# Performance work log

Measured on AMD Instinct MI355X. Metric: run time of the kernel, lower is better.

Reference implementation:

```python
import jax, jax.numpy as jnp
import numpy as np

EMBED_DIM = 1024
NUM_HEADS = 16
HEAD_DIM = EMBED_DIM // NUM_HEADS
CACHE_LEN = 16384


def setup_inputs() -> dict:
    key = jax.random.key(0)
    ks = jax.random.split(key, 10)
    s = 1.0 / np.sqrt(EMBED_DIM)
    return {
        "x": jax.random.normal(ks[0], (EMBED_DIM,), dtype=jnp.float32),
        "vk_cache": jax.random.normal(ks[1], (2, CACHE_LEN, NUM_HEADS, HEAD_DIM), dtype=jnp.float32),
        "Wv": jax.random.normal(ks[2], (EMBED_DIM, EMBED_DIM), dtype=jnp.float32) * s,
        "bv": jnp.zeros((EMBED_DIM,), dtype=jnp.float32),
        "Wq": jax.random.normal(ks[3], (EMBED_DIM, EMBED_DIM), dtype=jnp.float32) * s,
        "bq": jnp.zeros((EMBED_DIM,), dtype=jnp.float32),
        "Wk": jax.random.normal(ks[4], (EMBED_DIM, EMBED_DIM), dtype=jnp.float32) * s,
        "bk": jnp.zeros((EMBED_DIM,), dtype=jnp.float32),
        "Wo": jax.random.normal(ks[5], (EMBED_DIM, EMBED_DIM), dtype=jnp.float32) * s,
        "bo": jnp.zeros((EMBED_DIM,), dtype=jnp.float32),
    }


def reference(x, vk_cache, Wv, bv, Wq, bq, Wk, bk, Wo, bo):
    # Project single token to q/k/v
    v_i = (x @ Wv + bv).reshape(1, NUM_HEADS, HEAD_DIM)
    q_i = (x @ Wq + bq).reshape(NUM_HEADS, HEAD_DIM)
    k_i = (x @ Wk + bk).reshape(1, NUM_HEADS, HEAD_DIM)
    # Shift cache left by one, append new token   -> (CACHE_LEN, H, D)
    v = jnp.concatenate((vk_cache[0, 1:], v_i), axis=0)
    k = jnp.concatenate((vk_cache[1, 1:], k_i), axis=0)
    # Valid positions = any nonzero value entry
    mask = jnp.any(v != 0, axis=(1, 2))  # (CACHE_LEN,)
    # Scaled dot-product attention for the single query
    att = jnp.einsum('hd,khd->hk', q_i, k) / jnp.sqrt(jnp.float32(HEAD_DIM))
    att = jnp.where(mask, att, -jnp.inf)
    att = jax.nn.softmax(att, axis=-1)
    values = jnp.einsum('hk,khd->hd', att, v).reshape(EMBED_DIM)
    out_i = values @ Wo + bo
    return (out_i, jnp.stack([v, k]))
```

## Files before the change

### kernel.cpp

```cpp
#include <hip/hip_runtime.h>
#include <math.h>

#define EMBED 1024
#define NHEAD 16
#define HDIM  64
#define CLEN  16384

#define WS_QKV   0
#define WS_QP    3072
#define WS_PM    199680
#define WS_PL    216064
#define WS_PACC  232448
#define WS_GM    1281024
#define WS_GL    1281536
#define WS_GACC  1282048
#define WS_OPART 1314816

__global__ __launch_bounds__(256) void qkv_proj(
    const float* __restrict__ x,
    const float* __restrict__ Wq,
    const float* __restrict__ Wk,
    const float* __restrict__ Wv,
    float* __restrict__ ws) {
  int m = blockIdx.x >> 6;
  int c = blockIdx.x & 63;
  const float* W = (m == 0) ? Wq : (m == 1) ? Wk : Wv;
  int j = threadIdx.x << 2;
  int i0 = c * 16;
  float4 acc = make_float4(0.f, 0.f, 0.f, 0.f);
  for (int i = i0; i < i0 + 16; ++i) {
    float xv = x[i];
    float4 w = *(const float4*)(W + (size_t)i * EMBED + j);
    acc.x += xv * w.x; acc.y += xv * w.y;
    acc.z += xv * w.z; acc.w += xv * w.w;
  }
  *(float4*)(ws + WS_QP + (size_t)(m * 64 + c) * EMBED + j) = acc;
}

__global__ __launch_bounds__(256) void qkv_reduce(
    const float* __restrict__ bq, const float* __restrict__ bk,
    const float* __restrict__ bv, float* __restrict__ ws) {
  int m = blockIdx.x >> 2;
  int j = ((blockIdx.x & 3) << 8) + threadIdx.x;
  const float* b = (m == 0) ? bq : (m == 1) ? bk : bv;
  float s = b[j];
  const float* p = ws + WS_QP + (size_t)m * 64 * EMBED + j;
  for (int c = 0; c < 64; ++c) s += p[(size_t)c * EMBED];
  ws[WS_QKV + m * EMBED + j] = s;
}

__global__ __launch_bounds__(256) void shift_attn(
    const float* __restrict__ cache,
    float* __restrict__ out,
    float* __restrict__ ws) {
  __shared__ float sacc[3][EMBED];
  __shared__ float sm[4][NHEAD];
  __shared__ float sl[4][NHEAD];

  const int wv   = threadIdx.x >> 6;
  const int lane = threadIdx.x & 63;
  const int grp  = lane >> 4;

  float qf[16];
#pragma unroll
  for (int c = 0; c < 4; ++c) {
    float4 t = *(const float4*)(ws + WS_QKV + c * 256 + lane * 4);
    qf[c * 4] = t.x; qf[c * 4 + 1] = t.y; qf[c * 4 + 2] = t.z; qf[c * 4 + 3] = t.w;
  }

  float m[4] = {-INFINITY, -INFINITY, -INFINITY, -INFINITY};
  float l[4] = {0.f, 0.f, 0.f, 0.f};
  float acc[16];
#pragma unroll
  for (int j = 0; j < 16; ++j) acc[j] = 0.f;

  const float* vin = cache;
  const float* kin = cache + (size_t)CLEN * EMBED;
  float* vout = out + EMBED;
  float* kout = out + EMBED + (size_t)CLEN * EMBED;
  const int t0 = blockIdx.x * 16 + wv * 4;

  for (int it = 0; it < 4; ++it) {
    int t = t0 + it;
    const float* vsrc = (t < CLEN - 1) ? (vin + (size_t)(t + 1) * EMBED)
                                       : (ws + WS_QKV + 2 * EMBED);
    const float* ksrc = (t < CLEN - 1) ? (kin + (size_t)(t + 1) * EMBED)
                                       : (ws + WS_QKV + EMBED);
    float vv[16], kk[16];
#pragma unroll
    for (int c = 0; c < 4; ++c) {
      float4 tv = *(const float4*)(vsrc + c * 256 + lane * 4);
      vv[c * 4] = tv.x; vv[c * 4 + 1] = tv.y; vv[c * 4 + 2] = tv.z; vv[c * 4 + 3] = tv.w;
    }
#pragma unroll
    for (int c = 0; c < 4; ++c) {
      float4 tk = *(const float4*)(ksrc + c * 256 + lane * 4);
      kk[c * 4] = tk.x; kk[c * 4 + 1] = tk.y; kk[c * 4 + 2] = tk.z; kk[c * 4 + 3] = tk.w;
    }
    float* vd = vout + (size_t)t * EMBED;
    float* kd = kout + (size_t)t * EMBED;
#pragma unroll
    for (int c = 0; c < 4; ++c)
      *(float4*)(vd + c * 256 + lane * 4) =
          make_float4(vv[c * 4], vv[c * 4 + 1], vv[c * 4 + 2], vv[c * 4 + 3]);
#pragma unroll
    for (int c = 0; c < 4; ++c)
      *(float4*)(kd + c * 256 + lane * 4) =
          make_float4(kk[c * 4], kk[c * 4 + 1], kk[c * 4 + 2], kk[c * 4 + 3]);

    bool nz = false;
#pragma unroll
    for (int j = 0; j < 16; ++j) nz = nz || (vv[j] != 0.f);

    float d[4];
#pragma unroll
    for (int c = 0; c < 4; ++c) {
      d[c] = qf[c * 4] * kk[c * 4] + qf[c * 4 + 1] * kk[c * 4 + 1] +
             qf[c * 4 + 2] * kk[c * 4 + 2] + qf[c * 4 + 3] * kk[c * 4 + 3];
    }
#pragma unroll
    for (int msk = 1; msk <= 8; msk <<= 1) {
#pragma unroll
      for (int c = 0; c < 4; ++c) d[c] += __shfl_xor(d[c], msk, 64);
    }

    if (__any((int)nz)) {
#pragma unroll
      for (int c = 0; c < 4; ++c) {
        float s  = d[c] * 0.125f;
        float mn = fmaxf(m[c], s);
        float alpha = __expf(m[c] - mn);
        float p     = __expf(s - mn);
        l[c] = l[c] * alpha + p;
#pragma unroll
        for (int j = 0; j < 4; ++j)
          acc[c * 4 + j] = acc[c * 4 + j] * alpha + p * vv[c * 4 + j];
        m[c] = mn;
      }
    }
  }

  if (wv > 0) {
#pragma unroll
    for (int c = 0; c < 4; ++c)
      *(float4*)(&sacc[wv - 1][c * 256 + lane * 4]) =
          make_float4(acc[c * 4], acc[c * 4 + 1], acc[c * 4 + 2], acc[c * 4 + 3]);
    if ((lane & 15) == 0) {
#pragma unroll
      for (int c = 0; c < 4; ++c) {
        sm[wv][c * 4 + grp] = m[c];
        sl[wv][c * 4 + grp] = l[c];
      }
    }
  }
  __syncthreads();
  if (wv == 0) {
    for (int w = 1; w < 4; ++w) {
#pragma unroll
      for (int c = 0; c < 4; ++c) {
        float m2 = sm[w][c * 4 + grp];
        float M  = fmaxf(m[c], m2);
        float a1 = (m[c] == -INFINITY) ? 0.f : __expf(m[c] - M);
        float a2 = (m2   == -INFINITY) ? 0.f : __expf(m2 - M);
        l[c] = a1 * l[c] + a2 * sl[w][c * 4 + grp];
        float4 av = *(const float4*)(&sacc[w - 1][c * 256 + lane * 4]);
        acc[c * 4]     = a1 * acc[c * 4]     + a2 * av.x;
        acc[c * 4 + 1] = a1 * acc[c * 4 + 1] + a2 * av.y;
        acc[c * 4 + 2] = a1 * acc[c * 4 + 2] + a2 * av.z;
        acc[c * 4 + 3] = a1 * acc[c * 4 + 3] + a2 * av.w;
        m[c] = M;
      }
    }
    if ((lane & 15) == 0) {
#pragma unroll
      for (int c = 0; c < 4; ++c) {
        ws[WS_PM + blockIdx.x * NHEAD + c * 4 + grp] = m[c];
        ws[WS_PL + blockIdx.x * NHEAD + c * 4 + grp] = l[c];
      }
    }
    float* pa = ws + WS_PACC + (size_t)blockIdx.x * EMBED;
#pragma unroll
    for (int c = 0; c < 4; ++c)
      *(float4*)(pa + c * 256 + lane * 4) =
          make_float4(acc[c * 4], acc[c * 4 + 1], acc[c * 4 + 2], acc[c * 4 + 3]);
  }
}

__global__ __launch_bounds__(1024) void combine1(float* __restrict__ ws) {
  int g = blockIdx.x, t = threadIdx.x, h = t >> 6;
  int w0 = g * 32;
  float M = -INFINITY;
  for (int w = w0; w < w0 + 32; ++w)
    M = fmaxf(M, ws[WS_PM + w * NHEAD + h]);
  float L = 0.f, a = 0.f;
  for (int w = w0; w < w0 + 32; ++w) {
    float mw = ws[WS_PM + w * NHEAD + h];
    float sc = (mw == -INFINITY) ? 0.f : __expf(mw - M);
    L += sc * ws[WS_PL + w * NHEAD + h];
    a += sc * ws[WS_PACC + (size_t)w * EMBED + t];
  }
  if ((t & 63) == 0) {
    ws[WS_GM + g * NHEAD + h] = M;
    ws[WS_GL + g * NHEAD + h] = L;
  }
  ws[WS_GACC + (size_t)g * EMBED + t] = a;
}

__global__ __launch_bounds__(256) void out_proj(
    const float* __restrict__ Wo,
    float* __restrict__ ws) {
  __shared__ float svals[16];
  int c = blockIdx.x;
  int i0 = c * 16;
  int h0 = i0 >> 6;
  if (threadIdx.x < 16) {
    int i = i0 + threadIdx.x;
    float M = -INFINITY;
    for (int g = 0; g < 32; ++g)
      M = fmaxf(M, ws[WS_GM + g * NHEAD + h0]);
    float L = 0.f, a = 0.f;
    for (int g = 0; g < 32; ++g) {
      float mg = ws[WS_GM + g * NHEAD + h0];
      float sc = (mg == -INFINITY) ? 0.f : __expf(mg - M);
      L += sc * ws[WS_GL + g * NHEAD + h0];
      a += sc * ws[WS_GACC + (size_t)g * EMBED + i];
    }
    svals[threadIdx.x] = a / L;
  }
  __syncthreads();
  int j = threadIdx.x << 2;
  float4 acc = make_float4(0.f, 0.f, 0.f, 0.f);
  for (int i = 0; i < 16; ++i) {
    float xv = svals[i];
    float4 w = *(const float4*)(Wo + (size_t)(i0 + i) * EMBED + j);
    acc.x += xv * w.x; acc.y += xv * w.y;
    acc.z += xv * w.z; acc.w += xv * w.w;
  }
  *(float4*)(ws + WS_OPART + (size_t)c * EMBED + j) = acc;
}

__global__ __launch_bounds__(1024) void out_reduce(
    const float* __restrict__ ws, const float* __restrict__ bo,
    float* __restrict__ out) {
  int t = threadIdx.x;
  float s = bo[t];
  const float* p = ws + WS_OPART + t;
  for (int c = 0; c < 64; ++c) s += p[(size_t)c * EMBED];
  out[t] = s;
}

extern "C" void kernel_launch(void* const* d_in, const int* in_sizes, int n_in,
                              void* d_out, int out_size, void* d_ws, size_t ws_size,
                              hipStream_t stream) {
  const float* x     = (const float*)d_in[0];
  const float* cache = (const float*)d_in[1];
  const float* Wv    = (const float*)d_in[2];
  const float* bv    = (const float*)d_in[3];
  const float* Wq    = (const float*)d_in[4];
  const float* bq    = (const float*)d_in[5];
  const float* Wk    = (const float*)d_in[6];
  const float* bk    = (const float*)d_in[7];
  const float* Wo    = (const float*)d_in[8];
  const float* bo    = (const float*)d_in[9];
  float* out = (float*)d_out;
  float* ws  = (float*)d_ws;

  qkv_proj  <<<192, 256, 0, stream>>>(x, Wq, Wk, Wv, ws);
  qkv_reduce<<<12, 256, 0, stream>>>(bq, bk, bv, ws);
  shift_attn<<<1024, 256, 0, stream>>>(cache, out, ws);
  combine1  <<<32, 1024, 0, stream>>>(ws);
  out_proj  <<<64, 256, 0, stream>>>(Wo, ws);
  out_reduce<<<1, 1024, 0, stream>>>(ws, bo, out);
}
```

Measured before the change: 291.4 us.

## Split cache shift copy into separate blocks from attention compute

Removes the per-token shifted stores of the V/K cache from the attention blocks and launches 1024 extra blocks in the same kernel that do a flat, coalesced float4 copy of each cache plane, shifted by one row, plus the new token row. Attention blocks now only read and compute, and the copy blocks run alongside them. The cost is that the cache is read twice, once by the attention blocks and once by the copy blocks, which adds roughly 128 MB of extra read traffic, though some of it may hit in cache.

Measured after the change: 304.2 us. 1.04x slower.

```diff
diff --git a/kernel.cpp b/kernel.cpp
--- a/kernel.cpp
+++ b/kernel.cpp
@@ -57,6 +57,32 @@
   __shared__ float sm[4][NHEAD];
   __shared__ float sl[4][NHEAD];
 
+  const int bid = blockIdx.x;
+
+  if (bid >= 1024) {
+    const int cb    = bid - 1024;
+    const int plane = cb >> 9;
+    const int cbi   = cb & 511;
+    const int tid   = threadIdx.x;
+    const float* src = cache + (size_t)plane * CLEN * EMBED + EMBED;
+    float* dst = out + EMBED + (size_t)plane * CLEN * EMBED;
+    const int NT = 512 * 256;
+#pragma unroll 4
+    for (int i = 0; i < 32; ++i) {
+      size_t e4 = (size_t)i * NT + cbi * 256 + tid;
+      if (e4 < 4194048u) {
+        size_t e = e4 * 4;
+        *(float4*)(dst + e) = *(const float4*)(src + e);
+      }
+    }
+    if (cbi == 0 && tid < 256) {
+      const float* tok = ws + WS_QKV + (plane == 0 ? 2 * EMBED : EMBED);
+      *(float4*)(dst + (size_t)(CLEN - 1) * EMBED + tid * 4) =
+          *(const float4*)(tok + tid * 4);
+    }
+    return;
+  }
+
   const int wv   = threadIdx.x >> 6;
   const int lane = threadIdx.x & 63;
   const int grp  = lane >> 4;
@@ -76,9 +102,7 @@
 
   const float* vin = cache;
   const float* kin = cache + (size_t)CLEN * EMBED;
-  float* vout = out + EMBED;
-  float* kout = out + EMBED + (size_t)CLEN * EMBED;
-  const int t0 = blockIdx.x * 16 + wv * 4;
+  const int t0 = bid * 16 + wv * 4;
 
   for (int it = 0; it < 4; ++it) {
     int t = t0 + it;
@@ -97,16 +121,6 @@
       float4 tk = *(const float4*)(ksrc + c * 256 + lane * 4);
       kk[c * 4] = tk.x; kk[c * 4 + 1] = tk.y; kk[c * 4 + 2] = tk.z; kk[c * 4 + 3] = tk.w;
     }
-    float* vd = vout + (size_t)t * EMBED;
-    float* kd = kout + (size_t)t * EMBED;
-#pragma unroll
-    for (int c = 0; c < 4; ++c)
-      *(float4*)(vd + c * 256 + lane * 4) =
-          make_float4(vv[c * 4], vv[c * 4 + 1], vv[c * 4 + 2], vv[c * 4 + 3]);
-#pragma unroll
-    for (int c = 0; c < 4; ++c)
-      *(float4*)(kd + c * 256 + lane * 4) =
-          make_float4(kk[c * 4], kk[c * 4 + 1], kk[c * 4 + 2], kk[c * 4 + 3]);
 
     bool nz = false;
 #pragma unroll
@@ -174,11 +188,11 @@
     if ((lane & 15) == 0) {
 #pragma unroll
       for (int c = 0; c < 4; ++c) {
-        ws[WS_PM + blockIdx.x * NHEAD + c * 4 + grp] = m[c];
-        ws[WS_PL + blockIdx.x * NHEAD + c * 4 + grp] = l[c];
-      }
-    }
-    float* pa = ws + WS_PACC + (size_t)blockIdx.x * EMBED;
+        ws[WS_PM + bid * NHEAD + c * 4 + grp] = m[c];
+        ws[WS_PL + bid * NHEAD + c * 4 + grp] = l[c];
+      }
+    }
+    float* pa = ws + WS_PACC + (size_t)bid * EMBED;
 #pragma unroll
     for (int c = 0; c < 4; ++c)
       *(float4*)(pa + c * 256 + lane * 4) =
@@ -267,7 +281,7 @@
 
   qkv_proj  <<<192, 256, 0, stream>>>(x, Wq, Wk, Wv, ws);
   qkv_reduce<<<12, 256, 0, stream>>>(bq, bk, bv, ws);
-  shift_attn<<<1024, 256, 0, stream>>>(cache, out, ws);
+  shift_attn<<<2048, 256, 0, stream>>>(cache, out, ws);
   combine1  <<<32, 1024, 0, stream>>>(ws);
   out_proj  <<<64, 256, 0, stream>>>(Wo, ws);
   out_reduce<<<1, 1024, 0, stream>>>(ws, bo, out);
```
